# Kernel tuning notes

Measured on AMD Instinct MI355X. Metric: run time of the kernel, lower is better.

Reference implementation:

```python
import jax, jax.numpy as jnp
import numpy as np

NUM_RBF = 64
CUTOFF = 5.0
N_GRAPHS = 64


def _rbf_expand(d):
    # Gaussian RBF expansion on [0, CUTOFF] with cosine cutoff envelope.
    mus = jnp.linspace(0.0, CUTOFF, NUM_RBF, dtype=d.dtype)  # [M]
    gamma = (NUM_RBF / CUTOFF) ** 2  # 1 / spacing^2
    fc = 0.5 * (jnp.cos(jnp.pi * d / CUTOFF) + 1.0) * (d < CUTOFF)  # [E]
    return jnp.exp(-gamma * (d[:, None] - mus[None, :]) ** 2) * fc[:, None]  # [E,M]


def setup_inputs() -> dict:
    key = jax.random.key(0)
    k0, k1, k2, k3, k4, k5 = jax.random.split(key, 6)
    N, E, T = 50000, 1600000, 25
    pos = jax.random.normal(k0, (N, 3), jnp.float32) * 3.0
    edge_index = jax.random.randint(k1, (2, E), 0, N)
    atom_types = jax.random.randint(k2, (N,), 0, T)
    batch = jnp.sort(jax.random.randint(k3, (N,), 0, N_GRAPHS))
    rbf_params = jax.random.normal(k4, (T, T, NUM_RBF), jnp.float32)
    radial_filters = jax.random.uniform(k5, (T, T, NUM_RBF), jnp.float32)
    return {
        "pos": pos,
        "rbf_params": rbf_params,
        "radial_filters": radial_filters,
        "edge_index": edge_index,
        "atom_types": atom_types,
        "batch": batch,
    }


def reference(pos, rbf_params, radial_filters, edge_index, atom_types, batch):
    src, dst = edge_index[0], edge_index[1]
    # distances (no cell shifts)
    diff = pos[dst] - pos[src]                       # [E,3]
    d = jnp.sqrt(jnp.sum(diff * diff, axis=-1) + 1e-12)  # [E]
    # type-pair lookup with canonical ordering (sender <= receiver)
    s = atom_types[src]
    r = atom_types[dst]
    lo = jnp.minimum(s, r)
    hi = jnp.maximum(s, r)
    params = rbf_params[lo, hi]        # [E,M]
    filt = radial_filters[lo, hi]      # [E,M] (already in [0,1])
    expn = _rbf_expand(d) * filt       # filtered RBF expansion
    e_edge = jnp.sum(expn * params, axis=1)  # [E]
    # reduce per-edge energies to per-graph energies
    bmap = batch[src]
    energy = jax.ops.segment_sum(e_edge, bmap, num_segments=N_GRAPHS)  # [G]
    return energy
```

## Files before the change

kernel.cpp:

```cpp
#include <hip/hip_runtime.h>
#include <math.h>

#define NUM_RBF 64
#define N_GRAPHS 64

typedef int   int4v   __attribute__((ext_vector_type(4)));
typedef float float4v __attribute__((ext_vector_type(4)));


__global__ __launch_bounds__(256) void prologue_kernel(
    const float4v* __restrict__ p, const float4v* __restrict__ f,
    float4v* __restrict__ C, int n4,
    const float* __restrict__ pos, const int* __restrict__ types,
    const int* __restrict__ batch, float4v* __restrict__ rec, int N)
{
    int i = blockIdx.x * blockDim.x + threadIdx.x;
    if (i < n4) C[i] = p[i] * f[i];
    if (i < N) {
        int bits = (types[i] & 0xFF) | ((batch[i] & 0xFF) << 8);
        float4v r = { pos[3 * i], pos[3 * i + 1], pos[3 * i + 2],
                      __int_as_float(bits) };
        rec[i] = r;
    }
}

#define CUTOFF_F      5.0f
#define GAMMA_F       163.84f
#define SPACING_F     (float)(5.0 / 63.0)
#define INV_SPACING_F (float)(63.0 / 5.0)
#define PI_OVER_C_F   (float)(3.14159265358979323846 / 5.0)
#define TWO_GAMMA_S_F (float)(2.0 * 163.84 * 5.0 / 63.0)
#define LN_V          (-(64.0 / 63.0) * (64.0 / 63.0))
#define V_1           (float)exp(LN_V)
#define V_2           (float)exp(2.0 * LN_V)

__device__ __forceinline__ void edge_body(
    float4v rs, float4v rd, const float4v* __restrict__ C4, int T,
    float* __restrict__ bins)
{
    const float dx = rd.x - rs.x;
    const float dy = rd.y - rs.y;
    const float dz = rd.z - rs.z;
    const float d  = sqrtf(dx * dx + dy * dy + dz * dz + 1e-12f);
    if (d >= CUTOFF_F) return;

    const int sb = __float_as_int(rs.w);
    const int db = __float_as_int(rd.w);
    const int ts = sb & 0xFF;
    const int td = db & 0xFF;
    const int lo = min(ts, td);
    const int hi = max(ts, td);
    const int base = (lo * T + hi) * NUM_RBF;

    const float c = d * INV_SPACING_F;
    int a0 = ((int)floorf(c - 3.5f)) & ~3;
    a0 = max(0, min(NUM_RBF - 12, a0));

    const float4v* w = C4 + ((base + a0) >> 2);
    const float4v w0 = w[0], w1 = w[1], w2 = w[2];

    const float delta = d - (float)a0 * SPACING_F;
    const float d5 = delta - 5.0f * SPACING_F;
    const float t5 = __expf(-GAMMA_F * d5 * d5);
    const float x  = TWO_GAMMA_S_F * d5;
    const float u  = __expf(x);
    const float ui = __expf(-x);

    float acc = w1.y * t5;
    float t = t5, m = u * V_1;
    t *= m;  acc += w1.z * t;  m *= V_2;
    t *= m;  acc += w1.w * t;  m *= V_2;
    t *= m;  acc += w2.x * t;  m *= V_2;
    t *= m;  acc += w2.y * t;  m *= V_2;
    t *= m;  acc += w2.z * t;  m *= V_2;
    t *= m;  acc += w2.w * t;
    t = t5;  m = ui * V_1;
    t *= m;  acc += w1.x * t;  m *= V_2;
    t *= m;  acc += w0.w * t;  m *= V_2;
    t *= m;  acc += w0.z * t;  m *= V_2;
    t *= m;  acc += w0.y * t;  m *= V_2;
    t *= m;  acc += w0.x * t;

    const float fc = 0.5f * (__cosf(PI_OVER_C_F * d) + 1.0f);
    atomicAdd(&bins[(sb >> 8) & 0xFF], acc * fc);
}

__global__ __launch_bounds__(256) void edge_energy_kernel(
    const int*     __restrict__ edge_index,
    const float4v* __restrict__ rec,
    const float4v* __restrict__ C4,
    float*         __restrict__ partial,
    int E, int T)
{
    __shared__ float bins[N_GRAPHS];
    for (int i = threadIdx.x; i < N_GRAPHS; i += blockDim.x) bins[i] = 0.0f;
    __syncthreads();

    const int nfull  = E >> 2;
    const int stride = gridDim.x * blockDim.x;
    const int gid    = blockIdx.x * blockDim.x + threadIdx.x;

    for (int q = gid; q < nfull; q += stride) {
        const int e0 = q << 2;
        const int4v sv = __builtin_nontemporal_load(
            (const int4v*)(edge_index + e0));
        const int4v tv = __builtin_nontemporal_load(
            (const int4v*)(edge_index + E + e0));

        const float4v rs0 = rec[sv.x], rd0 = rec[tv.x];
        const float4v rs1 = rec[sv.y], rd1 = rec[tv.y];
        const float4v rs2 = rec[sv.z], rd2 = rec[tv.z];
        const float4v rs3 = rec[sv.w], rd3 = rec[tv.w];

        edge_body(rs0, rd0, C4, T, bins);
        edge_body(rs1, rd1, C4, T, bins);
        edge_body(rs2, rd2, C4, T, bins);
        edge_body(rs3, rd3, C4, T, bins);
    }

    if (gid == 0) {
        for (int e = nfull << 2; e < E; ++e) {
            const float4v rs = rec[edge_index[e]];
            const float4v rd = rec[edge_index[E + e]];
            edge_body(rs, rd, C4, T, bins);
        }
    }

    __syncthreads();
    for (int i = threadIdx.x; i < N_GRAPHS; i += blockDim.x)
        partial[blockIdx.x * N_GRAPHS + i] = bins[i];
}

__global__ __launch_bounds__(256) void reduce_kernel(
    const float* __restrict__ partial, float* __restrict__ out, int nblocks)
{
    const int g = blockIdx.x;
    float s = 0.0f;
    for (int i = threadIdx.x; i < nblocks; i += blockDim.x)
        s += partial[i * N_GRAPHS + g];

    for (int off = 32; off > 0; off >>= 1)
        s += __shfl_down(s, off, 64);

    __shared__ float red[4];
    const int wave = threadIdx.x >> 6;
    const int lane = threadIdx.x & 63;
    if (lane == 0) red[wave] = s;
    __syncthreads();
    if (threadIdx.x == 0)
        out[g] = red[0] + red[1] + red[2] + red[3];
}

extern "C" void kernel_launch(void* const* d_in, const int* in_sizes, int n_in,
                              void* d_out, int out_size, void* d_ws, size_t ws_size,
                              hipStream_t stream) {
    const float* pos            = (const float*)d_in[0];
    const float* rbf_params     = (const float*)d_in[1];
    const float* radial_filters = (const float*)d_in[2];
    const int*   edge_index     = (const int*)d_in[3];
    const int*   atom_types     = (const int*)d_in[4];
    const int*   batch          = (const int*)d_in[5];
    float*       out            = (float*)d_out;

    const int E = in_sizes[3] / 2;
    const int N = in_sizes[4];
    int T = 1;
    while ((T + 1) * (T + 1) * NUM_RBF <= in_sizes[1]) ++T;
    const int tbl_elems = T * T * NUM_RBF;

    float*   Ctab    = (float*)d_ws;
    float4v* recs    = (float4v*)((char*)d_ws + ((size_t)tbl_elems * 4 + 255) / 256 * 256);
    float*   partial = (float*)((char*)recs + (size_t)N * 16);

    const int nq = E >> 2;
    int nblocks = (nq + 255) / 256;
    const size_t part_off = (size_t)((char*)partial - (char*)d_ws);
    const size_t avail = (ws_size > part_off) ? (ws_size - part_off) : 0;
    const int maxb = (int)(avail / (N_GRAPHS * sizeof(float)));
    if (nblocks > maxb) nblocks = maxb > 0 ? maxb : 1;
    if (nblocks < 1) nblocks = 1;

    const int pro_n = max(tbl_elems / 4, N);
    prologue_kernel<<<(pro_n + 255) / 256, 256, 0, stream>>>(
        (const float4v*)rbf_params, (const float4v*)radial_filters,
        (float4v*)Ctab, tbl_elems / 4, pos, atom_types, batch, recs, N);
    edge_energy_kernel<<<nblocks, 256, 0, stream>>>(
        edge_index, recs, (const float4v*)Ctab, partial, E, T);
    reduce_kernel<<<N_GRAPHS, 256, 0, stream>>>(partial, out, nblocks);
}
```

Measured before the change: 96.39 us.

## Stage coefficient table in LDS with persistent 1024-thread blocks and prefetched first batch

```diff
diff --git a/kernel.cpp b/kernel.cpp
--- a/kernel.cpp
+++ b/kernel.cpp
@@ -35,7 +35,7 @@
 #define V_2           (float)exp(2.0 * LN_V)
 
 __device__ __forceinline__ void edge_body(
-    float4v rs, float4v rd, const float4v* __restrict__ C4, int T,
+    float4v rs, float4v rd, const float4v* __restrict__ tab, int T,
     float* __restrict__ bins)
 {
     const float dx = rd.x - rs.x;
@@ -56,7 +56,7 @@
     int a0 = ((int)floorf(c - 3.5f)) & ~3;
     a0 = max(0, min(NUM_RBF - 12, a0));
 
-    const float4v* w = C4 + ((base + a0) >> 2);
+    const float4v* w = tab + ((base + a0) >> 2);
     const float4v w0 = w[0], w1 = w[1], w2 = w[2];
 
     const float delta = d - (float)a0 * SPACING_F;
@@ -85,44 +85,73 @@
     atomicAdd(&bins[(sb >> 8) & 0xFF], acc * fc);
 }
 
-__global__ __launch_bounds__(256) void edge_energy_kernel(
+template<bool TAB_LDS>
+__global__ __launch_bounds__(1024) void edge_energy_kernel(
     const int*     __restrict__ edge_index,
     const float4v* __restrict__ rec,
     const float4v* __restrict__ C4,
     float*         __restrict__ partial,
-    int E, int T)
+    int E, int T, int tbl4)
 {
     __shared__ float bins[N_GRAPHS];
-    for (int i = threadIdx.x; i < N_GRAPHS; i += blockDim.x) bins[i] = 0.0f;
-    __syncthreads();
-
-    const int nfull  = E >> 2;
+    extern __shared__ float4v tab4[];
+
+    const int nq     = E >> 2;
     const int stride = gridDim.x * blockDim.x;
     const int gid    = blockIdx.x * blockDim.x + threadIdx.x;
 
-    for (int q = gid; q < nfull; q += stride) {
+    for (int i = threadIdx.x; i < N_GRAPHS; i += blockDim.x) bins[i] = 0.0f;
+
+    const int  q0   = gid;
+    const bool has0 = q0 < nq;
+    int4v sv = {0,0,0,0}, tv = {0,0,0,0};
+    float4v rs0{}, rd0{}, rs1{}, rd1{}, rs2{}, rd2{}, rs3{}, rd3{};
+    if (has0) {
+        const int e0 = q0 << 2;
+        sv = __builtin_nontemporal_load((const int4v*)(edge_index + e0));
+        tv = __builtin_nontemporal_load((const int4v*)(edge_index + E + e0));
+        rs0 = rec[sv.x]; rd0 = rec[tv.x];
+        rs1 = rec[sv.y]; rd1 = rec[tv.y];
+        rs2 = rec[sv.z]; rd2 = rec[tv.z];
+        rs3 = rec[sv.w]; rd3 = rec[tv.w];
+    }
+    if constexpr (TAB_LDS) {
+        for (int i = threadIdx.x; i < tbl4; i += blockDim.x)
+            tab4[i] = C4[i];
+    }
+    __syncthreads();
+
+    const float4v* tp;
+    if constexpr (TAB_LDS) tp = tab4; else tp = C4;
+
+    if (has0) {
+        edge_body(rs0, rd0, tp, T, bins);
+        edge_body(rs1, rd1, tp, T, bins);
+        edge_body(rs2, rd2, tp, T, bins);
+        edge_body(rs3, rd3, tp, T, bins);
+    }
+
+    for (int q = q0 + stride; q < nq; q += stride) {
         const int e0 = q << 2;
-        const int4v sv = __builtin_nontemporal_load(
+        const int4v s2 = __builtin_nontemporal_load(
             (const int4v*)(edge_index + e0));
-        const int4v tv = __builtin_nontemporal_load(
+        const int4v t2 = __builtin_nontemporal_load(
             (const int4v*)(edge_index + E + e0));
-
-        const float4v rs0 = rec[sv.x], rd0 = rec[tv.x];
-        const float4v rs1 = rec[sv.y], rd1 = rec[tv.y];
-        const float4v rs2 = rec[sv.z], rd2 = rec[tv.z];
-        const float4v rs3 = rec[sv.w], rd3 = rec[tv.w];
-
-        edge_body(rs0, rd0, C4, T, bins);
-        edge_body(rs1, rd1, C4, T, bins);
-        edge_body(rs2, rd2, C4, T, bins);
-        edge_body(rs3, rd3, C4, T, bins);
+        const float4v a0 = rec[s2.x], b0 = rec[t2.x];
+        const float4v a1 = rec[s2.y], b1 = rec[t2.y];
+        const float4v a2 = rec[s2.z], b2 = rec[t2.z];
+        const float4v a3 = rec[s2.w], b3 = rec[t2.w];
+        edge_body(a0, b0, tp, T, bins);
+        edge_body(a1, b1, tp, T, bins);
+        edge_body(a2, b2, tp, T, bins);
+        edge_body(a3, b3, tp, T, bins);
     }
 
     if (gid == 0) {
-        for (int e = nfull << 2; e < E; ++e) {
+        for (int e = nq << 2; e < E; ++e) {
             const float4v rs = rec[edge_index[e]];
             const float4v rd = rec[edge_index[E + e]];
-            edge_body(rs, rd, C4, T, bins);
+            edge_body(rs, rd, tp, T, bins);
         }
     }
 
@@ -167,13 +196,25 @@
     int T = 1;
     while ((T + 1) * (T + 1) * NUM_RBF <= in_sizes[1]) ++T;
     const int tbl_elems = T * T * NUM_RBF;
+    const int tbl4      = tbl_elems / 4;
+    const size_t tbl_bytes = (size_t)tbl_elems * sizeof(float);
 
     float*   Ctab    = (float*)d_ws;
-    float4v* recs    = (float4v*)((char*)d_ws + ((size_t)tbl_elems * 4 + 255) / 256 * 256);
+    float4v* recs    = (float4v*)((char*)d_ws + (tbl_bytes + 255) / 256 * 256);
     float*   partial = (float*)((char*)recs + (size_t)N * 16);
 
+    static int lds_ok = -1;
+    if (lds_ok < 0) {
+        auto fn = edge_energy_kernel<true>;
+        lds_ok = (tbl_bytes <= 160 * 1024 - 1024 &&
+                  hipFuncSetAttribute((const void*)fn,
+                      hipFuncAttributeMaxDynamicSharedMemorySize,
+                      (int)tbl_bytes) == hipSuccess) ? 1 : 0;
+    }
+
     const int nq = E >> 2;
-    int nblocks = (nq + 255) / 256;
+    int nblocks = (nq + 1023) / 1024;
+    if (nblocks > 256) nblocks = 256;
     const size_t part_off = (size_t)((char*)partial - (char*)d_ws);
     const size_t avail = (ws_size > part_off) ? (ws_size - part_off) : 0;
     const int maxb = (int)(avail / (N_GRAPHS * sizeof(float)));
@@ -184,7 +225,13 @@
     prologue_kernel<<<(pro_n + 255) / 256, 256, 0, stream>>>(
         (const float4v*)rbf_params, (const float4v*)radial_filters,
         (float4v*)Ctab, tbl_elems / 4, pos, atom_types, batch, recs, N);
-    edge_energy_kernel<<<nblocks, 256, 0, stream>>>(
-        edge_index, recs, (const float4v*)Ctab, partial, E, T);
+
+    if (lds_ok)
+        edge_energy_kernel<true><<<nblocks, 1024, tbl_bytes, stream>>>(
+            edge_index, recs, (const float4v*)Ctab, partial, E, T, tbl4);
+    else
+        edge_energy_kernel<false><<<nblocks, 1024, 0, stream>>>(
+            edge_index, recs, (const float4v*)Ctab, partial, E, T, tbl4);
+
     reduce_kernel<<<N_GRAPHS, 256, 0, stream>>>(partial, out, nblocks);
 }
```

Result: no change. 98.11 us (+1.8%).

## Software-pipeline edge gathers across grid-stride iterations and shrink grid

Applied to the files above, without the earlier changes.

```diff
diff --git a/kernel.cpp b/kernel.cpp
--- a/kernel.cpp
+++ b/kernel.cpp
@@ -35,7 +35,7 @@
 #define V_2           (float)exp(2.0 * LN_V)
 
 __device__ __forceinline__ void edge_body(
-    float4v rs, float4v rd, const float4v* __restrict__ C4, int T,
+    float4v rs, float4v rd, const float4v* __restrict__ tab, int T,
     float* __restrict__ bins)
 {
     const float dx = rd.x - rs.x;
@@ -56,8 +56,10 @@
     int a0 = ((int)floorf(c - 3.5f)) & ~3;
     a0 = max(0, min(NUM_RBF - 12, a0));
 
-    const float4v* w = C4 + ((base + a0) >> 2);
-    const float4v w0 = w[0], w1 = w[1], w2 = w[2];
+    const float4v* w = tab + ((base + a0) >> 2);
+    const float4v w0 = __builtin_nontemporal_load(w);
+    const float4v w1 = __builtin_nontemporal_load(w + 1);
+    const float4v w2 = __builtin_nontemporal_load(w + 2);
 
     const float delta = d - (float)a0 * SPACING_F;
     const float d5 = delta - 5.0f * SPACING_F;
@@ -85,6 +87,28 @@
     atomicAdd(&bins[(sb >> 8) & 0xFF], acc * fc);
 }
 
+struct Quad {
+    float4v rs0, rd0, rs1, rd1, rs2, rd2, rs3, rd3;
+};
+
+__device__ __forceinline__ Quad load_quad(
+    const int* __restrict__ ei, const float4v* __restrict__ rec,
+    int E, int e0)
+{
+    const int4v sv = __builtin_nontemporal_load((const int4v*)(ei + e0));
+    const int4v tv = __builtin_nontemporal_load((const int4v*)(ei + E + e0));
+    Quad g;
+    g.rs0 = __builtin_nontemporal_load(rec + sv.x);
+    g.rd0 = __builtin_nontemporal_load(rec + tv.x);
+    g.rs1 = __builtin_nontemporal_load(rec + sv.y);
+    g.rd1 = __builtin_nontemporal_load(rec + tv.y);
+    g.rs2 = __builtin_nontemporal_load(rec + sv.z);
+    g.rd2 = __builtin_nontemporal_load(rec + tv.z);
+    g.rs3 = __builtin_nontemporal_load(rec + sv.w);
+    g.rd3 = __builtin_nontemporal_load(rec + tv.w);
+    return g;
+}
+
 __global__ __launch_bounds__(256) void edge_energy_kernel(
     const int*     __restrict__ edge_index,
     const float4v* __restrict__ rec,
@@ -96,30 +120,31 @@
     for (int i = threadIdx.x; i < N_GRAPHS; i += blockDim.x) bins[i] = 0.0f;
     __syncthreads();
 
-    const int nfull  = E >> 2;
+    const int nq     = E >> 2;
     const int stride = gridDim.x * blockDim.x;
     const int gid    = blockIdx.x * blockDim.x + threadIdx.x;
 
-    for (int q = gid; q < nfull; q += stride) {
-        const int e0 = q << 2;
-        const int4v sv = __builtin_nontemporal_load(
-            (const int4v*)(edge_index + e0));
-        const int4v tv = __builtin_nontemporal_load(
-            (const int4v*)(edge_index + E + e0));
-
-        const float4v rs0 = rec[sv.x], rd0 = rec[tv.x];
-        const float4v rs1 = rec[sv.y], rd1 = rec[tv.y];
-        const float4v rs2 = rec[sv.z], rd2 = rec[tv.z];
-        const float4v rs3 = rec[sv.w], rd3 = rec[tv.w];
-
-        edge_body(rs0, rd0, C4, T, bins);
-        edge_body(rs1, rd1, C4, T, bins);
-        edge_body(rs2, rd2, C4, T, bins);
-        edge_body(rs3, rd3, C4, T, bins);
+    int  q   = gid;
+    bool has = q < nq;
+    Quad A;
+    if (has) A = load_quad(edge_index, rec, E, q << 2);
+
+    while (has) {
+        const int  qn   = q + stride;
+        const bool hasn = qn < nq;
+        Quad B = A;
+        if (hasn) B = load_quad(edge_index, rec, E, qn << 2);
+
+        edge_body(A.rs0, A.rd0, C4, T, bins);
+        edge_body(A.rs1, A.rd1, C4, T, bins);
+        edge_body(A.rs2, A.rd2, C4, T, bins);
+        edge_body(A.rs3, A.rd3, C4, T, bins);
+
+        A = B; q = qn; has = hasn;
     }
 
     if (gid == 0) {
-        for (int e = nfull << 2; e < E; ++e) {
+        for (int e = nq << 2; e < E; ++e) {
             const float4v rs = rec[edge_index[e]];
             const float4v rd = rec[edge_index[E + e]];
             edge_body(rs, rd, C4, T, bins);
@@ -173,7 +198,7 @@
     float*   partial = (float*)((char*)recs + (size_t)N * 16);
 
     const int nq = E >> 2;
-    int nblocks = (nq + 255) / 256;
+    int nblocks = (nq / 3 + 255) / 256;
     const size_t part_off = (size_t)((char*)partial - (char*)d_ws);
     const size_t avail = (ws_size > part_off) ? (ws_size - part_off) : 0;
     const int maxb = (int)(avail / (N_GRAPHS * sizeof(float)));
```

After: 103.5 us. 1.07x slower.
